# Performance work log

Hardware: AMD Instinct MI355X
Metric: run time of the kernel (lower is better)

Reference implementation:

```python
import jax, jax.numpy as jnp
import numpy as np

B, N, L = 64, 512, 768
M, K, H = 24, 30, 1024


def setup_inputs() -> dict:
    key = jax.random.key(0)
    ks = jax.random.split(key, 7)
    sent_embedding = jax.random.normal(ks[0], (B, N, L), dtype=jnp.float32)
    entity_embedding = jax.random.normal(ks[1], (B, M, K, H), dtype=jnp.float32)
    entity_embedding_mask = jax.random.bernoulli(ks[2], 0.1, (B, M, K))
    # -1 denotes a padded (absent) alias, as handled by select_alias_word_sent
    start_span_idx = jax.random.randint(ks[3], (B, M), -1, N, dtype=jnp.int32)
    end_span_idx = jax.random.randint(ks[4], (B, M), -1, N, dtype=jnp.int32)
    W_span = jax.random.normal(ks[5], (2 * L, H), dtype=jnp.float32) * (1.0 / np.sqrt(2 * L))
    b_span = jnp.zeros((H,), dtype=jnp.float32)
    return {
        "sent_embedding": sent_embedding,
        "entity_embedding": entity_embedding,
        "entity_embedding_mask": entity_embedding_mask,
        "start_span_idx": start_span_idx,
        "end_span_idx": end_span_idx,
        "W_span": W_span,
        "b_span": b_span,
    }


def _select_alias_word_sent(idx, sent):
    # idx: (B, M) positions into sentence; -1 means padded alias -> zero vector
    pad = idx == -1                                   # (B, M)
    safe = jnp.where(pad, 0, idx)                     # (B, M)
    g = jnp.take_along_axis(sent, safe[:, :, None], axis=1)  # (B, M, L)
    return jnp.where(pad[:, :, None], 0.0, g)


def reference(sent_embedding, entity_embedding, entity_embedding_mask,
              start_span_idx, end_span_idx, W_span, b_span):
    # gather start/end word vectors of each alias span
    start_w = _select_alias_word_sent(start_span_idx, sent_embedding)  # (B, M, L)
    end_w = _select_alias_word_sent(end_span_idx, sent_embedding)      # (B, M, L)
    pair = jnp.concatenate([start_w, end_w], axis=-1)                  # (B, M, 2L)
    # span_proj: single linear layer 2L -> H
    alias_emb = pair @ W_span + b_span                                 # (B, M, H)
    # zero out masked candidates
    ent = jnp.where(entity_embedding_mask[..., None], 0.0, entity_embedding)  # (B,M,K,H)
    # per-candidate dot product (the tiny bmm in the original)
    final_scores = jnp.einsum("bmh,bmkh->bmk", alias_emb, ent)         # (B, M, K)
    return final_scores, ent
```

## Files before the change

kernel.cpp:

```cpp
#include <hip/hip_runtime.h>
#include <stdint.h>

#define B_   64
#define N_   512
#define L_   768
#define M_   24
#define K_   30
#define H_   1024
#define L2_  1536

__global__ void detect_mask_kernel(const uint32_t* __restrict__ mw,
                                   int* __restrict__ flag) {
    __shared__ int f;
    if (threadIdx.x == 0) f = 0;
    __syncthreads();
    int local = 0;
    const int nw = (B_ * M_ * K_) / 4;
    for (int i = threadIdx.x; i < nw; i += blockDim.x) {
        uint32_t v = mw[i];
        if (v != 0u && v != 1u && v != 0x3F800000u) local = 1;
    }
    if (local) f = 1;
    __syncthreads();
    if (threadIdx.x == 0) *flag = f;
}

__global__ __launch_bounds__(256) void span_gemm_kernel(
    const float* __restrict__ sent,
    const int*   __restrict__ sidx,
    const int*   __restrict__ eidx,
    const float* __restrict__ W,
    const float* __restrict__ bias,
    float*       __restrict__ alias_out) {

    __shared__ float As[16][64];
    __shared__ float Bs[16][64];
    __shared__ int   offS[64];
    __shared__ int   offE[64];

    const int tid = threadIdx.x;
    const int bm0 = blockIdx.y * 64;
    const int h0  = blockIdx.x * 64;

    if (tid < 64) {
        const int bm = bm0 + tid;
        const int b  = bm / M_;
        const int si = sidx[bm];
        const int ei = eidx[bm];
        offS[tid] = (si < 0) ? -1 : (b * N_ + si) * L_;
        offE[tid] = (ei < 0) ? -1 : (b * N_ + ei) * L_;
    }
    __syncthreads();

    float acc[4][4] = {};

    const int ar  = tid >> 2;
    const int akq = (tid & 3) * 4;
    const int bkr = tid >> 4;
    const int bc  = (tid & 15) * 4;
    const int ty  = tid >> 4;
    const int tx  = tid & 15;

    for (int l0 = 0; l0 < L2_; l0 += 16) {
        {
            const int lb = l0 + akq;
            int off, ll;
            if (lb < L_) { off = offS[ar]; ll = lb; }
            else         { off = offE[ar]; ll = lb - L_; }
            float4 v;
            if (off < 0) v = make_float4(0.f, 0.f, 0.f, 0.f);
            else         v = *reinterpret_cast<const float4*>(sent + off + ll);
            As[akq + 0][ar] = v.x;
            As[akq + 1][ar] = v.y;
            As[akq + 2][ar] = v.z;
            As[akq + 3][ar] = v.w;
        }
        {
            const float4 v = *reinterpret_cast<const float4*>(
                W + (size_t)(l0 + bkr) * H_ + h0 + bc);
            *reinterpret_cast<float4*>(&Bs[bkr][bc]) = v;
        }
        __syncthreads();

#pragma unroll
        for (int k = 0; k < 16; ++k) {
            const float4 av = *reinterpret_cast<const float4*>(&As[k][ty * 4]);
            const float4 bv = *reinterpret_cast<const float4*>(&Bs[k][tx * 4]);
            acc[0][0] += av.x * bv.x; acc[0][1] += av.x * bv.y;
            acc[0][2] += av.x * bv.z; acc[0][3] += av.x * bv.w;
            acc[1][0] += av.y * bv.x; acc[1][1] += av.y * bv.y;
            acc[1][2] += av.y * bv.z; acc[1][3] += av.y * bv.w;
            acc[2][0] += av.z * bv.x; acc[2][1] += av.z * bv.y;
            acc[2][2] += av.z * bv.z; acc[2][3] += av.z * bv.w;
            acc[3][0] += av.w * bv.x; acc[3][1] += av.w * bv.y;
            acc[3][2] += av.w * bv.z; acc[3][3] += av.w * bv.w;
        }
        __syncthreads();
    }

    const float4 bb = *reinterpret_cast<const float4*>(bias + h0 + tx * 4);
#pragma unroll
    for (int i = 0; i < 4; ++i) {
        const int bm = bm0 + ty * 4 + i;
        const float4 o = make_float4(acc[i][0] + bb.x, acc[i][1] + bb.y,
                                     acc[i][2] + bb.z, acc[i][3] + bb.w);
        *reinterpret_cast<float4*>(alias_out + (size_t)bm * H_ + h0 + tx * 4) = o;
    }
}

__global__ __launch_bounds__(256) void ent_scores_kernel(
    const float* __restrict__ ent_in,
    const float* __restrict__ alias,
    const void*  __restrict__ mask,
    const int*   __restrict__ flag,
    float*       __restrict__ scores,
    float*       __restrict__ ent_out) {

    const int bmk = blockIdx.x;
    const int tid = threadIdx.x;

    const bool byte_packed = (*flag != 0);
    bool masked;
    if (byte_packed) masked = ((const uint8_t*)mask)[bmk] != 0;
    else             masked = ((const uint32_t*)mask)[bmk] != 0u;

    const size_t rowo = (size_t)bmk * H_;
    float p = 0.f;
    float4 e;
    if (masked) {
        e = make_float4(0.f, 0.f, 0.f, 0.f);
    } else {
        e = *reinterpret_cast<const float4*>(ent_in + rowo + tid * 4);
        const int bm = bmk / K_;
        const float4 a = *reinterpret_cast<const float4*>(
            alias + (size_t)bm * H_ + tid * 4);
        p = a.x * e.x + a.y * e.y + a.z * e.z + a.w * e.w;
    }
    *reinterpret_cast<float4*>(ent_out + rowo + tid * 4) = e;

#pragma unroll
    for (int off = 32; off > 0; off >>= 1) p += __shfl_down(p, off);
    __shared__ float red[4];
    if ((tid & 63) == 0) red[tid >> 6] = p;
    __syncthreads();
    if (tid == 0) scores[bmk] = red[0] + red[1] + red[2] + red[3];
}

extern "C" void kernel_launch(void* const* d_in, const int* in_sizes, int n_in,
                              void* d_out, int out_size, void* d_ws, size_t ws_size,
                              hipStream_t stream) {
    const float* sent = (const float*)d_in[0];
    const float* ent  = (const float*)d_in[1];
    const void*  mask = d_in[2];
    const int*   sidx = (const int*)d_in[3];
    const int*   eidx = (const int*)d_in[4];
    const float* W    = (const float*)d_in[5];
    const float* bias = (const float*)d_in[6];

    float* scores  = (float*)d_out;
    float* ent_out = (float*)d_out + (size_t)B_ * M_ * K_;

    int*   flag  = (int*)d_ws;
    float* alias = (float*)((char*)d_ws + 256);

    detect_mask_kernel<<<1, 256, 0, stream>>>((const uint32_t*)mask, flag);

    span_gemm_kernel<<<dim3(H_ / 64, (B_ * M_) / 64), 256, 0, stream>>>(
        sent, sidx, eidx, W, bias, alias);

    ent_scores_kernel<<<B_ * M_ * K_, 256, 0, stream>>>(
        ent, alias, mask, flag, scores, ent_out);
}
```

Measured before the change: 491.7 us.

## Route span GEMM through bf16 MFMA with gather and transposed-weight prep kernels

Adds a gather kernel that packs the start/end word vectors into a bf16 pair matrix, and a kernel that converts W to a transposed bf16 copy. A wave-level MFMA 16x16x32 bf16 GEMM then computes alias embeddings with fp32 accumulation, replacing the fp32 FMA tiled GEMM whenever the workspace is large enough. The intent is to cut the cost of the span projection GEMM by using the matrix cores. In exchange it adds two extra launches and re-converts W on every call. Rounding inputs to bf16 also lowers precision, which may push the scores against the tolerance. The dominant ent_scores streaming kernel is left unchanged.

```diff
diff --git a/kernel.cpp b/kernel.cpp
--- a/kernel.cpp
+++ b/kernel.cpp
@@ -8,6 +8,17 @@
 #define K_   30
 #define H_   1024
 #define L2_  1536
+#define BM_  (B_ * M_)
+#define BMK_ (B_ * M_ * K_)
+
+typedef __attribute__((ext_vector_type(8))) short bf16x8;
+typedef __attribute__((ext_vector_type(4))) float f32x4;
+
+__device__ __forceinline__ ushort f2bf(float f) {
+    union { float f; uint32_t u; } v; v.f = f;
+    uint32_t u = v.u + 0x7FFFu + ((v.u >> 16) & 1u);
+    return (ushort)(u >> 16);
+}
 
 __global__ void detect_mask_kernel(const uint32_t* __restrict__ mw,
                                    int* __restrict__ flag) {
@@ -15,7 +26,7 @@
     if (threadIdx.x == 0) f = 0;
     __syncthreads();
     int local = 0;
-    const int nw = (B_ * M_ * K_) / 4;
+    const int nw = BMK_ / 4;
     for (int i = threadIdx.x; i < nw; i += blockDim.x) {
         uint32_t v = mw[i];
         if (v != 0u && v != 1u && v != 0x3F800000u) local = 1;
@@ -23,6 +34,108 @@
     if (local) f = 1;
     __syncthreads();
     if (threadIdx.x == 0) *flag = f;
+}
+
+__global__ __launch_bounds__(192) void gather_pair_bf16(
+    const float* __restrict__ sent,
+    const int*   __restrict__ sidx,
+    const int*   __restrict__ eidx,
+    ushort*      __restrict__ pairB) {
+
+    const int bm = blockIdx.x;
+    const int t  = threadIdx.x;
+    const int l  = t * 8;
+    const int b  = bm / M_;
+
+    int idx, ll;
+    if (l < L_) { idx = sidx[bm]; ll = l; }
+    else        { idx = eidx[bm]; ll = l - L_; }
+
+    float4 v0 = make_float4(0.f, 0.f, 0.f, 0.f), v1 = v0;
+    if (idx >= 0) {
+        const float* src = sent + ((size_t)(b * N_ + idx)) * L_ + ll;
+        v0 = *reinterpret_cast<const float4*>(src);
+        v1 = *reinterpret_cast<const float4*>(src + 4);
+    }
+    ushort o[8] = { f2bf(v0.x), f2bf(v0.y), f2bf(v0.z), f2bf(v0.w),
+                    f2bf(v1.x), f2bf(v1.y), f2bf(v1.z), f2bf(v1.w) };
+    *reinterpret_cast<uint4*>(pairB + (size_t)bm * L2_ + l) =
+        *reinterpret_cast<const uint4*>(o);
+}
+
+__global__ __launch_bounds__(256) void wt_bf16_kernel(
+    const float* __restrict__ W, ushort* __restrict__ Wt) {
+
+    __shared__ ushort tile[32][33];
+    const int l0 = blockIdx.x * 32;
+    const int h0 = blockIdx.y * 32;
+    const int t  = threadIdx.x;
+
+    {
+        const int r  = t >> 3;
+        const int c4 = (t & 7) * 4;
+        const float4 v = *reinterpret_cast<const float4*>(
+            W + (size_t)(l0 + r) * H_ + h0 + c4);
+        tile[r][c4 + 0] = f2bf(v.x);
+        tile[r][c4 + 1] = f2bf(v.y);
+        tile[r][c4 + 2] = f2bf(v.z);
+        tile[r][c4 + 3] = f2bf(v.w);
+    }
+    __syncthreads();
+    {
+        const int hr = t >> 3;
+        const int l4 = (t & 7) * 4;
+        ushort4 o;
+        o.x = tile[l4 + 0][hr];
+        o.y = tile[l4 + 1][hr];
+        o.z = tile[l4 + 2][hr];
+        o.w = tile[l4 + 3][hr];
+        *reinterpret_cast<ushort4*>(Wt + (size_t)(h0 + hr) * L2_ + l0 + l4) = o;
+    }
+}
+
+__global__ __launch_bounds__(64) void mfma_span_gemm(
+    const ushort* __restrict__ pairB,
+    const ushort* __restrict__ WtB,
+    const float*  __restrict__ bias,
+    float*        __restrict__ alias_out) {
+
+    const int lane = threadIdx.x;
+    const int lr = lane & 15;
+    const int lg = lane >> 4;
+    const int c0 = blockIdx.x * 32;
+    const int r0 = blockIdx.y * 32;
+
+    f32x4 acc00 = {}, acc01 = {}, acc10 = {}, acc11 = {};
+
+    const ushort* a0 = pairB + (size_t)(r0 + lr) * L2_ + lg * 8;
+    const ushort* a1 = a0 + 16 * L2_;
+    const ushort* b0 = WtB   + (size_t)(c0 + lr) * L2_ + lg * 8;
+    const ushort* b1 = b0 + 16 * L2_;
+
+#pragma unroll 4
+    for (int k0 = 0; k0 < L2_; k0 += 32) {
+        const bf16x8 av0 = *reinterpret_cast<const bf16x8*>(a0 + k0);
+        const bf16x8 av1 = *reinterpret_cast<const bf16x8*>(a1 + k0);
+        const bf16x8 bv0 = *reinterpret_cast<const bf16x8*>(b0 + k0);
+        const bf16x8 bv1 = *reinterpret_cast<const bf16x8*>(b1 + k0);
+        acc00 = __builtin_amdgcn_mfma_f32_16x16x32_bf16(av0, bv0, acc00, 0, 0, 0);
+        acc01 = __builtin_amdgcn_mfma_f32_16x16x32_bf16(av0, bv1, acc01, 0, 0, 0);
+        acc10 = __builtin_amdgcn_mfma_f32_16x16x32_bf16(av1, bv0, acc10, 0, 0, 0);
+        acc11 = __builtin_amdgcn_mfma_f32_16x16x32_bf16(av1, bv1, acc11, 0, 0, 0);
+    }
+
+    const float bj0 = bias[c0 + lr];
+    const float bj1 = bias[c0 + 16 + lr];
+#pragma unroll
+    for (int q = 0; q < 4; ++q) {
+        const size_t rA = (size_t)(r0 + lg * 4 + q) * H_;
+        const size_t rB = (size_t)(r0 + 16 + lg * 4 + q) * H_;
+        alias_out[rA + c0 + lr]      = acc00[q] + bj0;
+        alias_out[rA + c0 + 16 + lr] = acc01[q] + bj1;
+        alias_out[rB + c0 + lr]      = acc10[q] + bj0;
+        alias_out[rB + c0 + 16 + lr] = acc11[q] + bj1;
+    }
 }
 
 __global__ __launch_bounds__(256) void span_gemm_kernel(
@@ -53,7 +166,6 @@
     __syncthreads();
 
     float acc[4][4] = {};
-
     const int ar  = tid >> 2;
     const int akq = (tid & 3) * 4;
     const int bkr = tid >> 4;
@@ -70,10 +182,8 @@
             float4 v;
             if (off < 0) v = make_float4(0.f, 0.f, 0.f, 0.f);
             else         v = *reinterpret_cast<const float4*>(sent + off + ll);
-            As[akq + 0][ar] = v.x;
-            As[akq + 1][ar] = v.y;
-            As[akq + 2][ar] = v.z;
-            As[akq + 3][ar] = v.w;
+            As[akq + 0][ar] = v.x;  As[akq + 1][ar] = v.y;
+            As[akq + 2][ar] = v.z;  As[akq + 3][ar] = v.w;
         }
         {
             const float4 v = *reinterpret_cast<const float4*>(
@@ -81,7 +191,6 @@
             *reinterpret_cast<float4*>(&Bs[bkr][bc]) = v;
         }
         __syncthreads();
-
 #pragma unroll
         for (int k = 0; k < 16; ++k) {
             const float4 av = *reinterpret_cast<const float4*>(&As[k][ty * 4]);
@@ -158,16 +267,29 @@
     const float* bias = (const float*)d_in[6];
 
     float* scores  = (float*)d_out;
-    float* ent_out = (float*)d_out + (size_t)B_ * M_ * K_;
-
-    int*   flag  = (int*)d_ws;
-    float* alias = (float*)((char*)d_ws + 256);
+    float* ent_out = (float*)d_out + (size_t)BMK_;
+
+    const size_t ALIAS_B = (size_t)BM_ * H_ * 4;
+    const size_t PAIR_B  = (size_t)BM_ * L2_ * 2;
+    const size_t WT_B    = (size_t)H_ * L2_ * 2;
+
+    int*    flag  = (int*)d_ws;
+    float*  alias = (float*)((char*)d_ws + 256);
+    ushort* pairB = (ushort*)((char*)d_ws + 256 + ALIAS_B);
+    ushort* WtB   = (ushort*)((char*)d_ws + 256 + ALIAS_B + PAIR_B);
 
     detect_mask_kernel<<<1, 256, 0, stream>>>((const uint32_t*)mask, flag);
 
-    span_gemm_kernel<<<dim3(H_ / 64, (B_ * M_) / 64), 256, 0, stream>>>(
-        sent, sidx, eidx, W, bias, alias);
-
-    ent_scores_kernel<<<B_ * M_ * K_, 256, 0, stream>>>(
+    if (ws_size >= 256 + ALIAS_B + PAIR_B + WT_B) {
+        gather_pair_bf16<<<BM_, 192, 0, stream>>>(sent, sidx, eidx, pairB);
+        wt_bf16_kernel<<<dim3(L2_ / 32, H_ / 32), 256, 0, stream>>>(W, WtB);
+        mfma_span_gemm<<<dim3(H_ / 32, BM_ / 32), 64, 0, stream>>>(
+            pairB, WtB, bias, alias);
+    } else {
+        span_gemm_kernel<<<dim3(H_ / 64, BM_ / 64), 256, 0, stream>>>(
+            sent, sidx, eidx, W, bias, alias);
+    }
+
+    ent_scores_kernel<<<BMK_, 256, 0, stream>>>(
         ent, alias, mask, flag, scores, ent_out);
 }
```

Result: faster. 419.8 us (-14.6%).
